# Kernel tuning notes

Measured on AMD Instinct MI355X. Metric: run time of the kernel, lower is better.

Reference implementation:

```python
import jax, jax.numpy as jnp
import numpy as np

B, T, D = 16, 512, 256
HH = D // 2   # per-direction hidden of bidirectional GRU
G, Z, R, NA = 32, 8, 16, 18


def _gru_step(h, x, wih, whh, bih, bhh):
    # torch.nn.GRUCell math
    gi = x @ wih.T + bih
    gh = h @ whh.T + bhh
    ir, iz, inn = jnp.split(gi, 3, axis=-1)
    hr, hz, hn = jnp.split(gh, 3, axis=-1)
    r = jax.nn.sigmoid(ir + hr)
    z = jax.nn.sigmoid(iz + hz)
    n = jnp.tanh(inn + r * hn)
    return (1.0 - z) * n + z * h


def _gru_seq(x_tbd, wih, whh, bih, bhh):
    h0 = jnp.zeros((x_tbd.shape[1], whh.shape[1]), x_tbd.dtype)
    def step(h, x):
        h = _gru_step(h, x, wih, whh, bih, bhh)
        return h, h
    _, hs = jax.lax.scan(step, h0, x_tbd)
    return hs  # (T, B, H)


def setup_inputs() -> dict:
    key = jax.random.key(0)
    ks = jax.random.split(key, 26)
    rn = lambda k, s, sc: jax.random.normal(k, s, jnp.float32) * sc
    d = {
        'e_seq': rn(ks[0], (B, T, D), 1.0),
        'eps':   rn(ks[1], (B, T, Z), 1.0),
        # acausal bidirectional GRU (fwd + bwd cells)
        'wih_f': rn(ks[2], (3 * HH, D), D ** -0.5),  'whh_f': rn(ks[3], (3 * HH, HH), HH ** -0.5),
        'bih_f': jnp.zeros((3 * HH,)), 'bhh_f': jnp.zeros((3 * HH,)),
        'wih_b': rn(ks[4], (3 * HH, D), D ** -0.5),  'whh_b': rn(ks[5], (3 * HH, HH), HH ** -0.5),
        'bih_b': jnp.zeros((3 * HH,)), 'bhh_b': jnp.zeros((3 * HH,)),
        # controller encoder GRUCell(2D -> G) + heads
        'wih_e': rn(ks[6], (3 * G, 2 * D), (2 * D) ** -0.5), 'whh_e': rn(ks[7], (3 * G, G), G ** -0.5),
        'bih_e': jnp.zeros((3 * G,)), 'bhh_e': jnp.zeros((3 * G,)),
        'mu_w': rn(ks[8], (Z, G), G ** -0.5),  'mu_b': jnp.zeros((Z,)),
        'lv_w': rn(ks[9], (Z, G), G ** -0.5),  'lv_b': jnp.zeros((Z,)),
        # switching unit MLP (D+G+Z -> 64 -> 1)
        'sw1_w': rn(ks[10], (64, D + G + Z), (D + G + Z) ** -0.5), 'sw1_b': jnp.zeros((64,)),
        'sw2_w': rn(ks[11], (1, 64), 64 ** -0.5), 'sw2_b': jnp.zeros((1,)),
        # decoder hypernet (Z -> 32 -> 2*D*R)
        'dec1_w': rn(ks[12], (32, Z), Z ** -0.5), 'dec1_b': jnp.zeros((32,)),
        'dec2_w': rn(ks[13], (2 * D * R, 32), 32 ** -0.5), 'dec2_b': jnp.zeros((2 * D * R,)),
        # final norm + action head
        'ln_g': jnp.ones((D,)), 'ln_b': jnp.zeros((D,)),
        'head_w': rn(ks[14], (NA, D), D ** -0.5), 'head_b': jnp.zeros((NA,)),
    }
    return d


def _forward(e_seq, eps, wih_f, whh_f, bih_f, bhh_f, wih_b, whh_b, bih_b, bhh_b,
             wih_e, whh_e, bih_e, bhh_e, mu_w, mu_b, lv_w, lv_b,
             sw1_w, sw1_b, sw2_w, sw2_b, dec1_w, dec1_b, dec2_w, dec2_b,
             ln_g, ln_b, head_w, head_b):
    Bz, Tt, Dm = e_seq.shape
    e_tbd = jnp.swapaxes(e_seq, 0, 1)                      # (T, B, D)
    # AcausalEmbedder: bidirectional GRU
    fwd = _gru_seq(e_tbd, wih_f, whh_f, bih_f, bhh_f)
    bwd = _gru_seq(e_tbd[::-1], wih_b, whh_b, bih_b, bhh_b)[::-1]
    s_tbd = jnp.concatenate([fwd, bwd], axis=-1)           # (T, B, D)
    eps_tbd = jnp.swapaxes(eps, 0, 1)

    h0 = jnp.zeros((Bz, whh_e.shape[1]), e_seq.dtype)
    z0 = jnp.zeros((Bz, mu_w.shape[0]), e_seq.dtype)

    def step(carry, xs):
        h, z_prev = carry
        e_t, s_t, eps_t = xs
        h = _gru_step(h, jnp.concatenate([e_t, s_t], axis=-1), wih_e, whh_e, bih_e, bhh_e)
        mu = h @ mu_w.T + mu_b
        logvar = h @ lv_w.T + lv_b
        # switching unit uses updated h (causal)
        hid = jnp.tanh(jnp.concatenate([e_t, h, z_prev], axis=-1) @ sw1_w.T + sw1_b)
        beta = jax.nn.sigmoid(hid @ sw2_w.T + sw2_b)       # (B, 1)
        z = beta * (mu + jnp.exp(0.5 * logvar) * eps_t) + (1.0 - beta) * z_prev
        return (h, jax.lax.stop_gradient(z)), (mu, logvar, beta, z)

    _, (mu_t, lv_t, be_t, z_t) = jax.lax.scan(step, (h0, z0), (e_tbd, s_tbd, eps_tbd))
    mu_seq = jnp.swapaxes(mu_t, 0, 1)
    logvar_seq = jnp.swapaxes(lv_t, 0, 1)
    beta_seq = jnp.swapaxes(be_t, 0, 1)
    z_seq = jnp.swapaxes(z_t, 0, 1)                        # (B, T, Z)

    # ControllerDecoder: z -> (A, Bm); apply U = A @ Bm^T without materializing U
    hmid = jnp.tanh(z_seq @ dec1_w.T + dec1_b)
    ab = hmid @ dec2_w.T + dec2_b                          # (B, T, 2*D*R)
    DR = ab.shape[-1] // 2
    A = ab[..., :DR].reshape(Bz, Tt, Dm, -1)               # (B, T, D, R)
    Bm = ab[..., DR:].reshape(Bz, Tt, Dm, -1)
    tmp = jnp.einsum('btdr,btd->btr', Bm, e_seq)
    perturbed = e_seq + jnp.einsum('btdr,btr->btd', A, tmp)

    # final LayerNorm + action head on obs positions
    mean = perturbed.mean(-1, keepdims=True)
    var = perturbed.var(-1, keepdims=True)
    xn = (perturbed - mean) * jax.lax.rsqrt(var + 1e-5) * ln_g + ln_b
    logits = xn @ head_w.T + head_b                        # (B, T, NA)
    return logits, mu_seq, logvar_seq, beta_seq, z_seq


def reference(e_seq, eps, wih_f, whh_f, bih_f, bhh_f, wih_b, whh_b, bih_b, bhh_b,
              wih_e, whh_e, bih_e, bhh_e, mu_w, mu_b, lv_w, lv_b,
              sw1_w, sw1_b, sw2_w, sw2_b, dec1_w, dec1_b, dec2_w, dec2_b,
              ln_g, ln_b, head_w, head_b):
    return _forward(e_seq, eps, wih_f, whh_f, bih_f, bhh_f, wih_b, whh_b, bih_b, bhh_b,
                    wih_e, whh_e, bih_e, bhh_e, mu_w, mu_b, lv_w, lv_b,
                    sw1_w, sw1_b, sw2_w, sw2_b, dec1_w, dec1_b, dec2_w, dec2_b,
                    ln_g, ln_b, head_w, head_b)
```

## Files before the change

### kernel.cpp

```cpp
#include <hip/hip_runtime.h>

#define TT 512
#define BB 16
#define DD 256
#define HHH 128
#define GG 32
#define ZZ 8
#define RR_ 16
#define NAA 18

typedef _Float16 h2v __attribute__((ext_vector_type(2)));
typedef __attribute__((ext_vector_type(4))) float f4;
typedef __attribute__((ext_vector_type(4))) int i4;

__device__ __forceinline__ float sigmoid_(float x) { return 1.f / (1.f + __expf(-x)); }
__device__ __forceinline__ float tanh_(float x) { float e = __expf(2.f * x); return 1.f - 2.f / (e + 1.f); }
__device__ __forceinline__ float dot4(float4 a, float4 b) {
    return a.x * b.x + a.y * b.y + a.z * b.z + a.w * b.w;
}
__device__ __forceinline__ h2v u2h2(unsigned u) { union { unsigned u; h2v h; } c; c.u = u; return c.h; }

__device__ __forceinline__ void lds_barrier() {
    asm volatile("s_waitcnt lgkmcnt(0)" ::: "memory");
    __builtin_amdgcn_s_barrier();
}

template <int CTRL, int RM, int BM, bool BC>
__device__ __forceinline__ float dpp_add_f(float v) {
    return v + __int_as_float(__builtin_amdgcn_update_dpp(0, __float_as_int(v), CTRL, RM, BM, BC));
}
__device__ __forceinline__ float wave_sum_bcast(float p) {
    p = dpp_add_f<0x111, 0xf, 0xf, true>(p);
    p = dpp_add_f<0x112, 0xf, 0xf, true>(p);
    p = dpp_add_f<0x114, 0xf, 0xf, true>(p);
    p = dpp_add_f<0x118, 0xf, 0xf, true>(p);
    p = dpp_add_f<0x142, 0xa, 0xf, false>(p);
    p = dpp_add_f<0x143, 0xc, 0xf, false>(p);
    return __int_as_float(__builtin_amdgcn_readlane(__float_as_int(p), 63));
}
__device__ __forceinline__ float quad_sum(float v) {
    v = dpp_add_f<0xB1, 0xf, 0xf, true>(v);
    v = dpp_add_f<0x4E, 0xf, 0xf, true>(v);
    return v;
}

__global__ __launch_bounds__(256) void pack_w(
    const float* __restrict__ wf, const float* __restrict__ wb,
    const float* __restrict__ we,
    unsigned* __restrict__ pk, unsigned* __restrict__ pk_e)
{
    int i = blockIdx.x * 256 + threadIdx.x;
    if (i < 49152) {
        int dir = i / 24576; int r = i % 24576;
        int w = r / 3072;    int r2 = r % 3072;
        int T = r2 / 1024;   int r3 = r2 % 1024;
        int kt = r3 / 256;   int r4 = r3 % 256;
        int lane = r4 / 4;   int jd = r4 % 4;
        const float* wsrc = dir ? wb : wf;
        int row = T * 128 + 16 * w + (lane & 15);
        int k0 = kt * 32 + (lane >> 4) * 8 + 2 * jd;
        union { _Float16 h[2]; unsigned u; } c;
        c.h[0] = (_Float16)wsrc[row * 128 + k0];
        c.h[1] = (_Float16)wsrc[row * 128 + k0 + 1];
        pk[i] = c.u;
    } else if (i < 50688) {
        int ie = i - 49152;
        int s = ie / 384;  int rem = ie % 384;
        int k = rem / 12;  int e = rem % 12;
        int j = e / 4;     int m = e % 4;
        int row = j * 32 + k, k0 = 8 * s + 2 * m;
        union { _Float16 h[2]; unsigned u; } c;
        c.h[0] = (_Float16)we[row * 32 + k0];
        c.h[1] = (_Float16)we[row * 32 + k0 + 1];
        pk_e[ie] = c.u;
    }
}

__global__ __launch_bounds__(256) void gemm_k(
    const float* __restrict__ A, int K, const float* __restrict__ W, int ldw,
    const float* __restrict__ bias, float* __restrict__ Out, int ldout, int N, int accFlag)
{
    __shared__ float At[64][36];
    __shared__ float Wt[32][36];
    int row0 = blockIdx.x * 64, n0 = blockIdx.y * 32;
    int tid = threadIdx.x;
    int tx = tid & 15, ty = tid >> 4;
    float acc[4][2] = {};
    for (int k0 = 0; k0 < K; k0 += 32) {
        #pragma unroll
        for (int i = 0; i < 8; ++i) {
            int idx = tid + i * 256; int rr = idx >> 5, kk = idx & 31;
            At[rr][kk] = A[(size_t)(row0 + rr) * K + k0 + kk];
        }
        #pragma unroll
        for (int i = 0; i < 4; ++i) {
            int idx = tid + i * 256; int nn = idx >> 5, kk = idx & 31;
            Wt[nn][kk] = (n0 + nn < N) ? W[(size_t)(n0 + nn) * ldw + k0 + kk] : 0.f;
        }
        __syncthreads();
        #pragma unroll
        for (int kk = 0; kk < 32; kk += 4) {
            float4 w0 = *(const float4*)&Wt[tx][kk];
            float4 w1 = *(const float4*)&Wt[tx + 16][kk];
            #pragma unroll
            for (int rr = 0; rr < 4; ++rr) {
                float4 av = *(const float4*)&At[ty * 4 + rr][kk];
                acc[rr][0] += dot4(av, w0);
                acc[rr][1] += dot4(av, w1);
            }
        }
        __syncthreads();
    }
    #pragma unroll
    for (int cc = 0; cc < 2; ++cc) {
        int n = n0 + tx + cc * 16;
        if (n < N) {
            float badd = bias ? bias[n] : 0.f;
            #pragma unroll
            for (int rr = 0; rr < 4; ++rr) {
                int row = row0 + ty * 4 + rr;
                float v = acc[rr][cc] + badd;
                if (accFlag) Out[(size_t)row * ldout + n] += v;
                else         Out[(size_t)row * ldout + n] = v;
            }
        }
    }
}

__global__ __launch_bounds__(256) void gemm_gi(
    const float* __restrict__ A,
    const float* __restrict__ wf, const float* __restrict__ bf, float* __restrict__ of,
    const float* __restrict__ wb, const float* __restrict__ bb, float* __restrict__ ob)
{
    __shared__ float At[64][36];
    __shared__ float Wt[32][36];
    int y = blockIdx.y;
    const float* W; const float* bias; float* Out; int n0;
    if (y < 12) { W = wf; bias = bf; Out = of; n0 = y * 32; }
    else        { W = wb; bias = bb; Out = ob; n0 = (y - 12) * 32; }
    int row0 = blockIdx.x * 64;
    int tid = threadIdx.x;
    int tx = tid & 15, ty = tid >> 4;
    float acc[4][2] = {};
    for (int k0 = 0; k0 < 256; k0 += 32) {
        #pragma unroll
        for (int i = 0; i < 8; ++i) {
            int idx = tid + i * 256; int rr = idx >> 5, kk = idx & 31;
            At[rr][kk] = A[(size_t)(row0 + rr) * 256 + k0 + kk];
        }
        #pragma unroll
        for (int i = 0; i < 4; ++i) {
            int idx = tid + i * 256; int nn = idx >> 5, kk = idx & 31;
            Wt[nn][kk] = W[(size_t)(n0 + nn) * 256 + k0 + kk];
        }
        __syncthreads();
        #pragma unroll
        for (int kk = 0; kk < 32; kk += 4) {
            float4 w0 = *(const float4*)&Wt[tx][kk];
            float4 w1 = *(const float4*)&Wt[tx + 16][kk];
            #pragma unroll
            for (int rr = 0; rr < 4; ++rr) {
                float4 av = *(const float4*)&At[ty * 4 + rr][kk];
                acc[rr][0] += dot4(av, w0);
                acc[rr][1] += dot4(av, w1);
            }
        }
        __syncthreads();
    }
    #pragma unroll
    for (int cc = 0; cc < 2; ++cc) {
        int n = n0 + tx + cc * 16;
        float badd = bias[n];
        #pragma unroll
        for (int rr = 0; rr < 4; ++rr) {
            int row = row0 + ty * 4 + rr;
            Out[(size_t)row * 384 + n] = acc[rr][cc] + badd;
        }
    }
}

struct __align__(16) SmGru { _Float16 hb[2][128]; };
struct __align__(16) SmGemm { float At[64][36]; float Wt[32][36]; };
union __align__(16) SmU { SmGru g; SmGemm m; };

__device__ __forceinline__ void gemm_tile512(
    const float* __restrict__ A, int K, const float* __restrict__ W, int ldw,
    const float* __restrict__ bias, float* __restrict__ Out, int ldout, int N,
    int row0, int n0, SmGemm& sm)
{
    int tid = threadIdx.x;
    int tx = tid & 31, ty = tid >> 5;
    float acc[4] = {};
    for (int k0 = 0; k0 < K; k0 += 32) {
        #pragma unroll
        for (int i = 0; i < 4; ++i) {
            int idx = tid + i * 512; int rr = idx >> 5, kk = idx & 31;
            sm.At[rr][kk] = A[(size_t)(row0 + rr) * K + k0 + kk];
        }
        #pragma unroll
        for (int i = 0; i < 2; ++i) {
            int idx = tid + i * 512; int nn = idx >> 5, kk = idx & 31;
            sm.Wt[nn][kk] = (n0 + nn < N) ? W[(size_t)(n0 + nn) * ldw + k0 + kk] : 0.f;
        }
        __syncthreads();
        #pragma unroll
        for (int kk = 0; kk < 32; kk += 4) {
            float4 w0 = *(const float4*)&sm.Wt[tx][kk];
            #pragma unroll
            for (int rr = 0; rr < 4; ++rr) {
                float4 av = *(const float4*)&sm.At[ty * 4 + rr][kk];
                acc[rr] += dot4(av, w0);
            }
        }
        __syncthreads();
    }
    int n = n0 + tx;
    if (n < N) {
        float badd = bias ? bias[n] : 0.f;
        #pragma unroll
        for (int rr = 0; rr < 4; ++rr)
            Out[(size_t)(row0 + ty * 4 + rr) * ldout + n] = acc[rr] + badd;
    }
}

__global__ __launch_bounds__(512, 2) void gru_fused(
    const float* __restrict__ gi_f, const float* __restrict__ gi_b,
    const unsigned* __restrict__ pk,
    const float* __restrict__ bhh_f, const float* __restrict__ bhh_b,
    float* __restrict__ s_seq,
    const float* __restrict__ e,
    const float* __restrict__ wih_e, const float* __restrict__ bih_e, float* __restrict__ gie,
    const float* __restrict__ sw1_w, const float* __restrict__ sw1_b, float* __restrict__ swe)
{
    __shared__ SmU sm;
    int bx = blockIdx.x;
    if (bx >= 416) {
        int t = bx - 416;
        gemm_tile512(e, 256, sw1_w, 296, sw1_b, swe, 64, 64, (t & 127) * 64, (t >> 7) * 32, sm.m);
        return;
    }
    if (bx >= 32) {
        int t = bx - 32;
        gemm_tile512(e, 256, wih_e, 512, bih_e, gie, 96, 96, (t & 127) * 64, (t >> 7) * 32, sm.m);
        return;
    }

    int dir = bx >> 4, b = bx & 15;
    const float* gi  = dir ? gi_b  : gi_f;
    const float* bhh = dir ? bhh_b : bhh_f;
    int tid = threadIdx.x;
    int w = tid >> 6;
    int lane = tid & 63;
    int quad = lane >> 4;
    int c = lane & 15;
    int j = 16 * w + c;

    i4 bf[3][4];
    #pragma unroll
    for (int T = 0; T < 3; ++T)
        #pragma unroll
        for (int kt = 0; kt < 4; ++kt)
            bf[T][kt] = *(const i4*)(pk + (size_t)((((dir * 8 + w) * 3 + T) * 4 + kt) * 64 + lane) * 4);
    #pragma unroll
    for (int T = 0; T < 3; ++T)
        #pragma unroll
        for (int kt = 0; kt < 4; ++kt)
            asm volatile("" : "+a"(bf[T][kt]));

    if (tid < 128) sm.g.hb[0][tid] = (_Float16)0.f;

    float bhr = 0.f, bhz = 0.f, bhn = 0.f;
    float gra = 0.f, gza = 0.f, gna = 0.f;
    float grb = 0.f, gzb = 0.f, gnb = 0.f;
    float hreg = 0.f;
    if (lane < 16) {
        bhr = bhh[j]; bhz = bhh[128 + j]; bhn = bhh[256 + j];
        int t0 = dir ? 511 : 0;
        int t1 = dir ? 510 : 1;
        size_t p0 = (size_t)(b * TT + t0) * 384;
        size_t p1 = (size_t)(b * TT + t1) * 384;
        gra = gi[p0 + j]; gza = gi[p0 + 128 + j]; gna = gi[p0 + 256 + j];
        grb = gi[p1 + j]; gzb = gi[p1 + 128 + j]; gnb = gi[p1 + 256 + j];
    }
    __syncthreads();

    int cur = 0;
    auto body = [&](int step, float& gr, float& gz, float& gn) {
        i4 af[4];
        #pragma unroll
        for (int kt = 0; kt < 4; ++kt)
            af[kt] = *(const i4*)(&sm.g.hb[cur][kt * 32 + quad * 8]);
        f4 accrA = {0.f, 0.f, 0.f, 0.f}, accrB = {0.f, 0.f, 0.f, 0.f};
        f4 acczA = {0.f, 0.f, 0.f, 0.f}, acczB = {0.f, 0.f, 0.f, 0.f};
        f4 accnA = {0.f, 0.f, 0.f, 0.f}, accnB = {0.f, 0.f, 0.f, 0.f};
        asm volatile("s_nop 3");
        asm volatile("v_mfma_f32_16x16x32_f16 %0, %1, %2, %0" : "+v"(accrA) : "v"(af[0]), "a"(bf[0][0]));
        asm volatile("v_mfma_f32_16x16x32_f16 %0, %1, %2, %0" : "+v"(acczA) : "v"(af[0]), "a"(bf[1][0]));
        asm volatile("v_mfma_f32_16x16x32_f16 %0, %1, %2, %0" : "+v"(accnA) : "v"(af[0]), "a"(bf[2][0]));
        asm volatile("v_mfma_f32_16x16x32_f16 %0, %1, %2, %0" : "+v"(accrB) : "v"(af[2]), "a"(bf[0][2]));
        asm volatile("v_mfma_f32_16x16x32_f16 %0, %1, %2, %0" : "+v"(acczB) : "v"(af[2]), "a"(bf[1][2]));
        asm volatile("v_mfma_f32_16x16x32_f16 %0, %1, %2, %0" : "+v"(accnB) : "v"(af[2]), "a"(bf[2][2]));
        asm volatile("v_mfma_f32_16x16x32_f16 %0, %1, %2, %0" : "+v"(accrA) : "v"(af[1]), "a"(bf[0][1]));
        asm volatile("v_mfma_f32_16x16x32_f16 %0, %1, %2, %0" : "+v"(acczA) : "v"(af[1]), "a"(bf[1][1]));
        asm volatile("v_mfma_f32_16x16x32_f16 %0, %1, %2, %0" : "+v"(accnA) : "v"(af[1]), "a"(bf[2][1]));
        asm volatile("v_mfma_f32_16x16x32_f16 %0, %1, %2, %0" : "+v"(accrB) : "v"(af[3]), "a"(bf[0][3]));
        asm volatile("v_mfma_f32_16x16x32_f16 %0, %1, %2, %0" : "+v"(acczB) : "v"(af[3]), "a"(bf[1][3]));
        asm volatile("v_mfma_f32_16x16x32_f16 %0, %1, %2, %0" : "+v"(accnB) : "v"(af[3]), "a"(bf[2][3]));
        asm volatile("s_nop 7\n\ts_nop 7");
        if (lane < 16) {
            int t = dir ? (511 - step) : step;
            int p = b * TT + t;
            float ar = accrA[0] + accrB[0];
            float az = acczA[0] + acczB[0];
            float an = accnA[0] + accnB[0];
            float r = sigmoid_(gr + bhr + ar);
            float z = sigmoid_(gz + bhz + az);
            float n = tanh_(gn + r * (bhn + an));
            float hn = (1.f - z) * n + z * hreg;
            hreg = hn;
            sm.g.hb[cur ^ 1][j] = (_Float16)hn;
            s_seq[(size_t)p * 256 + dir * 128 + j] = hn;
            int s2 = step + 2;
            int tp = (s2 < 512) ? (dir ? (511 - s2) : s2) : t;
            size_t p2 = (size_t)(b * TT + tp) * 384;
            gr = gi[p2 + j]; gz = gi[p2 + 128 + j]; gn = gi[p2 + 256 + j];
        }
        lds_barrier();
        cur ^= 1;
    };

    for (int step = 0; step < 512; step += 2) {
        body(step,     gra, gza, gna);
        body(step + 1, grb, gzb, gnb);
    }
}

__global__ __launch_bounds__(128, 1) void ctrl_fused(
    const float* __restrict__ gie, const unsigned* __restrict__ pk_e,
    const float* __restrict__ bhh_e,
    const float* __restrict__ mu_w, const float* __restrict__ mu_b,
    const float* __restrict__ lv_w, const float* __restrict__ lv_b,
    const float* __restrict__ sw1_w, const float* __restrict__ sw2_w,
    const float* __restrict__ sw2_b,
    const float* __restrict__ swe,
    const float* __restrict__ eps,
    float* __restrict__ out_mu, float* __restrict__ out_lv,
    float* __restrict__ beta_o, float* __restrict__ z_o)
{
    int b = blockIdx.x;
    int tid = threadIdx.x;
    int wid = tid >> 6;
    int lane = tid & 63;
    int pbase = b * TT;

    __shared__ __align__(16) _Float16 hb[2][32];
    __shared__ __align__(16) float    hf[2][32];
    __shared__ __align__(16) float    zc[8];

    int k = lane >> 1, s2 = lane & 1;
    unsigned wg[24];
    float bhr = 0.f, bhz = 0.f, bhn = 0.f, hreg = 0.f;
    float g1a = 0.f, g2a = 0.f, g3a = 0.f, g1b = 0.f, g2b = 0.f, g3b = 0.f;
    if (wid == 0) {
        #pragma unroll
        for (int ss = 0; ss < 2; ++ss) {
            const uint4* wp = (const uint4*)(pk_e + ((size_t)((2 * s2 + ss) * 32) + k) * 12);
            #pragma unroll
            for (int i = 0; i < 3; ++i) {
                uint4 u = wp[i];
                wg[12 * ss + 4 * i + 0] = u.x;
                wg[12 * ss + 4 * i + 1] = u.y;
                wg[12 * ss + 4 * i + 2] = u.z;
                wg[12 * ss + 4 * i + 3] = u.w;
            }
        }
        if (tid < 32) hb[0][tid] = (_Float16)0.f;
        if (s2 == 0) {
            bhr = bhh_e[k]; bhz = bhh_e[32 + k]; bhn = bhh_e[64 + k];
            size_t p0 = (size_t)pbase * 96, p1 = (size_t)(pbase + 1) * 96;
            g1a = gie[p0 + k]; g2a = gie[p0 + 32 + k]; g3a = gie[p0 + 64 + k];
            g1b = gie[p1 + k]; g2b = gie[p1 + 32 + k]; g3b = gie[p1 + 64 + k];
        }
    }

    int q = lane;
    int x = lane >> 3, kind = (lane >> 2) & 1, s = lane & 3;
    float swh[32], wz[8], mlw[8];
    float w2 = 0.f, sb2 = 0.f, mlb = 0.f;
    float zreg[8] = {0.f, 0.f, 0.f, 0.f, 0.f, 0.f, 0.f, 0.f};
    float hpa = 0.f, hpb = 0.f, epa = 0.f, epb = 0.f;
    if (wid == 1) {
        #pragma unroll
        for (int kk = 0; kk < 32; ++kk) swh[kk] = sw1_w[(size_t)q * 296 + 256 + kk];
        #pragma unroll
        for (int xx = 0; xx < 8; ++xx) wz[xx] = sw1_w[(size_t)q * 296 + 288 + xx];
        w2 = sw2_w[q];
        sb2 = sw2_b[0];
        const float* mw = kind ? lv_w : mu_w;
        #pragma unroll
        for (int m = 0; m < 8; ++m) mlw[m] = mw[x * 32 + 8 * s + m];
        mlb = kind ? lv_b[x] : mu_b[x];
        hpa = swe[(size_t)pbase * 64 + q];
        hpb = swe[(size_t)(pbase + 1) * 64 + q];
        epa = eps[(size_t)pbase * 8 + x];
        epb = eps[(size_t)(pbase + 1) * 8 + x];
    }
    __syncthreads();

    int cur = 0;

    auto prod = [&](int t, float& g1, float& g2, float& g3) {
        const uint4* hv = (const uint4*)(&hb[cur][16 * s2]);
        uint4 hA = hv[0], hB = hv[1];
        unsigned hw[8] = {hA.x, hA.y, hA.z, hA.w, hB.x, hB.y, hB.z, hB.w};
        float a0 = 0.f, a1 = 0.f, a2 = 0.f, c0 = 0.f, c1 = 0.f, c2 = 0.f;
        #pragma unroll
        for (int m = 0; m < 4; ++m) {
            a0 = __builtin_amdgcn_fdot2(u2h2(wg[m]),      u2h2(hw[m]),     a0, false);
            a1 = __builtin_amdgcn_fdot2(u2h2(wg[4 + m]),  u2h2(hw[m]),     a1, false);
            a2 = __builtin_amdgcn_fdot2(u2h2(wg[8 + m]),  u2h2(hw[m]),     a2, false);
            c0 = __builtin_amdgcn_fdot2(u2h2(wg[12 + m]), u2h2(hw[4 + m]), c0, false);
            c1 = __builtin_amdgcn_fdot2(u2h2(wg[16 + m]), u2h2(hw[4 + m]), c1, false);
            c2 = __builtin_amdgcn_fdot2(u2h2(wg[20 + m]), u2h2(hw[4 + m]), c2, false);
        }
        a0 += c0; a1 += c1; a2 += c2;
        a0 = dpp_add_f<0xB1, 0xf, 0xf, true>(a0);
        a1 = dpp_add_f<0xB1, 0xf, 0xf, true>(a1);
        a2 = dpp_add_f<0xB1, 0xf, 0xf, true>(a2);
        if (s2 == 0) {
            float r = sigmoid_(g1 + bhr + a0);
            float z = sigmoid_(g2 + bhz + a1);
            float n = tanh_(g3 + r * (bhn + a2));
            float hn = (1.f - z) * n + z * hreg;
            hreg = hn;
            hb[cur ^ 1][k] = (_Float16)hn;
            hf[cur ^ 1][k] = hn;
            int t2 = (t + 2 < 512) ? t + 2 : t;
            size_t p2 = (size_t)(pbase + t2) * 96;
            g1 = gie[p2 + k]; g2 = gie[p2 + 32 + k]; g3 = gie[p2 + 64 + k];
        }
    };

    auto cons = [&](int t, float& hp, float& ep) {
        const float4* hv4 = (const float4*)(&hf[cur][0]);
        float4 h4[8];
        #pragma unroll
        for (int i = 0; i < 8; ++i) h4[i] = hv4[i];
        float a = hp;
        #pragma unroll
        for (int xx = 0; xx < 8; ++xx) a += wz[xx] * zreg[xx];
        #pragma unroll
        for (int i = 0; i < 8; ++i) {
            a += swh[4 * i]     * h4[i].x;
            a += swh[4 * i + 1] * h4[i].y;
            a += swh[4 * i + 2] * h4[i].z;
            a += swh[4 * i + 3] * h4[i].w;
        }
        float hid = tanh_(a);
        float beta = sigmoid_(wave_sum_bcast(w2 * hid) + sb2);
        float4 hs0 = *(const float4*)(&hf[cur][8 * s]);
        float4 hs1 = *(const float4*)(&hf[cur][8 * s + 4]);
        float pacc = mlw[0] * hs0.x + mlw[1] * hs0.y + mlw[2] * hs0.z + mlw[3] * hs0.w
                   + mlw[4] * hs1.x + mlw[5] * hs1.y + mlw[6] * hs1.z + mlw[7] * hs1.w;
        pacc = quad_sum(pacc);
        float v = pacc + mlb;
        float other = __int_as_float(__builtin_amdgcn_ds_swizzle(__float_as_int(v), 0x101F));
        float muv = kind ? other : v;
        float lvv = kind ? v : other;
        float cand = muv + __expf(0.5f * lvv) * ep;
        if ((lane & 7) == 0) zc[x] = cand;
        asm volatile("s_waitcnt lgkmcnt(0)" ::: "memory");
        float4 cz0 = *(const float4*)&zc[0];
        float4 cz1 = *(const float4*)&zc[4];
        float omb = 1.f - beta;
        zreg[0] = beta * cz0.x + omb * zreg[0]; zreg[1] = beta * cz0.y + omb * zreg[1];
        zreg[2] = beta * cz0.z + omb * zreg[2]; zreg[3] = beta * cz0.w + omb * zreg[3];
        zreg[4] = beta * cz1.x + omb * zreg[4]; zreg[5] = beta * cz1.y + omb * zreg[5];
        zreg[6] = beta * cz1.z + omb * zreg[6]; zreg[7] = beta * cz1.w + omb * zreg[7];
        int p = pbase + t;
        if (lane == 0) {
            beta_o[p] = beta;
            *(float4*)(z_o + (size_t)p * 8)     = make_float4(zreg[0], zreg[1], zreg[2], zreg[3]);
            *(float4*)(z_o + (size_t)p * 8 + 4) = make_float4(zreg[4], zreg[5], zreg[6], zreg[7]);
        }
        if ((lane & 7) == 0) out_mu[(size_t)p * 8 + x] = muv;
        if ((lane & 7) == 4) out_lv[(size_t)p * 8 + x] = lvv;
        int t2 = (t + 2 < 512) ? t + 2 : t;
        hp = swe[(size_t)(pbase + t2) * 64 + q];
        ep = eps[(size_t)(pbase + t2) * 8 + x];
    };

    for (int it = 0; it < 512; it += 2) {
        if (wid == 0) prod(it, g1a, g2a, g3a);
        else if (it > 0) cons(it - 1, hpb, epb);
        lds_barrier();
        cur ^= 1;
        if (wid == 0) prod(it + 1, g1b, g2b, g3b);
        else cons(it, hpa, epa);
        lds_barrier();
        cur ^= 1;
    }
    if (wid == 1) cons(511, hpb, epb);
}

__global__ __launch_bounds__(256, 3) void decoder_final(
    const float* __restrict__ e_seq, const float* __restrict__ z_o,
    const float* __restrict__ dec1_w, const float* __restrict__ dec1_b,
    const float* __restrict__ dec2_w, const float* __restrict__ dec2_b,
    const float* __restrict__ ln_g, const float* __restrict__ ln_b,
    const float* __restrict__ head_w, const float* __restrict__ head_b,
    float* __restrict__ logits)
{
    __shared__ __align__(16) float e_l[8][256];
    __shared__ __align__(16) float hmid[8][32];
    __shared__ float zl[8][8];
    __shared__ float tmpw[8][16];
    __shared__ __align__(16) float partb[2048];
    __shared__ float red1[8][16];
    __shared__ float red2[8][16];
    __shared__ float stats[8][2];
    int tid = threadIdx.x;
    int p0 = blockIdx.x * 8;

    {
        const float4* eg = (const float4*)(e_seq + (size_t)p0 * 256);
        float4* el4 = (float4*)&e_l[0][0];
        el4[tid] = eg[tid];
        el4[tid + 256] = eg[tid + 256];
        if (tid < 64) ((float*)zl)[tid] = z_o[p0 * 8 + tid];
    }
    __syncthreads();
    {
        int pp = tid >> 5, g = tid & 31;
        float a = dec1_b[g];
        #pragma unroll
        for (int x = 0; x < 8; ++x) a += dec1_w[g * 8 + x] * zl[pp][x];
        hmid[pp][g] = tanh_(a);
    }
    __syncthreads();
    {
        int r = tid & 15, dgrp = tid >> 4;
        float acc[8];
        #pragma unroll
        for (int pp = 0; pp < 8; ++pp) acc[pp] = 0.f;
        for (int iblk = 0; iblk < 8; ++iblk) {
            float4 wr[2][8]; float wb[2]; int dd[2];
            #pragma unroll
            for (int ii = 0; ii < 2; ++ii) {
                int d = dgrp + 16 * (iblk * 2 + ii);
                dd[ii] = d;
                int row = 4096 + d * 16 + r;
                const float4* wp = (const float4*)(dec2_w + (size_t)row * 32);
                #pragma unroll
                for (int g = 0; g < 8; ++g) wr[ii][g] = wp[g];
                wb[ii] = dec2_b[row];
            }
            #pragma unroll 1
            for (int pp = 0; pp < 8; ++pp) {
                const float4* hv = (const float4*)hmid[pp];
                float b0 = wb[0], b1 = wb[1];
                #pragma unroll
                for (int g = 0; g < 8; ++g) {
                    float4 hh = hv[g];
                    b0 += dot4(wr[0][g], hh);
                    b1 += dot4(wr[1][g], hh);
                }
                acc[pp] += b0 * e_l[pp][dd[0]] + b1 * e_l[pp][dd[1]];
            }
        }
        #pragma unroll
        for (int pp = 0; pp < 8; ++pp) partb[(pp * 16 + r) * 16 + dgrp] = acc[pp];
    }
    __syncthreads();
    if (tid < 128) {
        int pp = tid >> 4, rr = tid & 15;
        float s = 0.f;
        #pragma unroll
        for (int dg = 0; dg < 16; ++dg) s += partb[(pp * 16 + rr) * 16 + dg];
        tmpw[pp][rr] = s;
    }
    __syncthreads();
    {
        int d = tid;
        float po[8];
        #pragma unroll
        for (int pp = 0; pp < 8; ++pp) po[pp] = e_l[pp][d];
        for (int rblk = 0; rblk < 8; ++rblk) {
            float4 wr[2][8]; float wb[2];
            #pragma unroll
            for (int ii = 0; ii < 2; ++ii) {
                int row = d * 16 + rblk * 2 + ii;
                const float4* wp = (const float4*)(dec2_w + (size_t)row * 32);
                #pragma unroll
                for (int g = 0; g < 8; ++g) wr[ii][g] = wp[g];
                wb[ii] = dec2_b[row];
            }
            #pragma unroll 1
            for (int pp = 0; pp < 8; ++pp) {
                const float4* hv = (const float4*)hmid[pp];
                float a0 = wb[0], a1 = wb[1];
                #pragma unroll
                for (int g = 0; g < 8; ++g) {
                    float4 hh = hv[g];
                    a0 += dot4(wr[0][g], hh);
                    a1 += dot4(wr[1][g], hh);
                }
                po[pp] += a0 * tmpw[pp][rblk * 2] + a1 * tmpw[pp][rblk * 2 + 1];
            }
        }
        #pragma unroll
        for (int pp = 0; pp < 8; ++pp) partb[pp * 256 + d] = po[pp];
    }
    __syncthreads();
    if (tid < 128) {
        int pp = tid >> 4, c = tid & 15;
        float s = 0.f, s2 = 0.f;
        #pragma unroll
        for (int i = 0; i < 16; ++i) { float v = partb[pp * 256 + c * 16 + i]; s += v; s2 += v * v; }
        red1[pp][c] = s; red2[pp][c] = s2;
    }
    __syncthreads();
    if (tid < 8) {
        float s = 0.f, s2 = 0.f;
        #pragma unroll
        for (int c = 0; c < 16; ++c) { s += red1[tid][c]; s2 += red2[tid][c]; }
        float mean = s * (1.f / 256.f);
        float var = s2 * (1.f / 256.f) - mean * mean;
        stats[tid][0] = mean;
        stats[tid][1] = rsqrtf(var + 1e-5f);
    }
    __syncthreads();
    {
        int d = tid;
        float g = ln_g[d], bln = ln_b[d];
        #pragma unroll
        for (int pp = 0; pp < 8; ++pp) {
            float v = (partb[pp * 256 + d] - stats[pp][0]) * stats[pp][1];
            partb[pp * 256 + d] = v * g + bln;
        }
    }
    __syncthreads();
    if (tid < 144) {
        int pp = tid / 18, na = tid - pp * 18;
        float a = head_b[na];
        for (int d2 = 0; d2 < 256; ++d2)
            a += partb[pp * 256 + d2] * head_w[na * 256 + d2];
        logits[(size_t)(p0 + pp) * 18 + na] = a;
    }
}

extern "C" void kernel_launch(void* const* d_in, const int* in_sizes, int n_in,
                              void* d_out, int out_size, void* d_ws, size_t ws_size,
                              hipStream_t stream) {
    (void)in_sizes; (void)n_in; (void)out_size; (void)ws_size;
    const float* e     = (const float*)d_in[0];
    const float* eps   = (const float*)d_in[1];
    const float* wih_f = (const float*)d_in[2];
    const float* whh_f = (const float*)d_in[3];
    const float* bih_f = (const float*)d_in[4];
    const float* bhh_f = (const float*)d_in[5];
    const float* wih_b = (const float*)d_in[6];
    const float* whh_b = (const float*)d_in[7];
    const float* bih_b = (const float*)d_in[8];
    const float* bhh_b = (const float*)d_in[9];
    const float* wih_e = (const float*)d_in[10];
    const float* whh_e = (const float*)d_in[11];
    const float* bih_e = (const float*)d_in[12];
    const float* bhh_e = (const float*)d_in[13];
    const float* mu_w  = (const float*)d_in[14];
    const float* mu_b  = (const float*)d_in[15];
    const float* lv_w  = (const float*)d_in[16];
    const float* lv_b  = (const float*)d_in[17];
    const float* sw1_w = (const float*)d_in[18];
    const float* sw1_b = (const float*)d_in[19];
    const float* sw2_w = (const float*)d_in[20];
    const float* sw2_b = (const float*)d_in[21];
    const float* dec1_w = (const float*)d_in[22];
    const float* dec1_b = (const float*)d_in[23];
    const float* dec2_w = (const float*)d_in[24];
    const float* dec2_b = (const float*)d_in[25];
    const float* ln_g  = (const float*)d_in[26];
    const float* ln_b  = (const float*)d_in[27];
    const float* head_w = (const float*)d_in[28];
    const float* head_b = (const float*)d_in[29];

    float* ws    = (float*)d_ws;
    float* gi_f  = ws;
    float* gi_b  = gi_f + 3145728;
    float* gie   = gi_b + 3145728;
    float* swe   = gie + 786432;
    float* s_seq = swe + 524288;
    float* h_seq = s_seq + 2097152;
    unsigned* pk   = (unsigned*)(h_seq + 262144);
    unsigned* pk_e = pk + 49152;
    (void)h_seq;

    float* out       = (float*)d_out;
    float* out_logit = out;
    float* out_mu    = out + 147456;
    float* out_lv    = out + 212992;
    float* out_beta  = out + 278528;
    float* out_z     = out + 286720;

    pack_w<<<198, 256, 0, stream>>>(whh_f, whh_b, whh_e, pk, pk_e);
    gemm_gi<<<dim3(128, 24), 256, 0, stream>>>(e, wih_f, bih_f, gi_f, wih_b, bih_b, gi_b);
    gru_fused<<<672, 512, 0, stream>>>(gi_f, gi_b, pk, bhh_f, bhh_b, s_seq,
                                       e, wih_e, bih_e, gie, sw1_w, sw1_b, swe);
    gemm_k<<<dim3(128, 3), 256, 0, stream>>>(s_seq, 256, wih_e + 256, 512, nullptr, gie, 96, 96, 1);
    ctrl_fused<<<16, 128, 0, stream>>>(gie, pk_e, bhh_e, mu_w, mu_b, lv_w, lv_b,
                                       sw1_w, sw2_w, sw2_b, swe, eps,
                                       out_mu, out_lv, out_beta, out_z);
    decoder_final<<<1024, 256, 0, stream>>>(e, out_z, dec1_w, dec1_b, dec2_w, dec2_b,
                                            ln_g, ln_b, head_w, head_b, out_logit);
}
```

Before: 1.005 ms.

## Batch four controller steps per barrier with an 8-slot hidden-state ring

```diff
diff --git a/kernel.cpp b/kernel.cpp
--- a/kernel.cpp
+++ b/kernel.cpp
@@ -42,6 +42,9 @@
     v = dpp_add_f<0xB1, 0xf, 0xf, true>(v);
     v = dpp_add_f<0x4E, 0xf, 0xf, true>(v);
     return v;
+}
+__device__ __forceinline__ float rdlane(float v, int l) {
+    return __int_as_float(__builtin_amdgcn_readlane(__float_as_int(v), l));
 }
 
 __global__ __launch_bounds__(256) void pack_w(
@@ -353,14 +356,13 @@
     int lane = tid & 63;
     int pbase = b * TT;
 
-    __shared__ __align__(16) _Float16 hb[2][32];
-    __shared__ __align__(16) float    hf[2][32];
-    __shared__ __align__(16) float    zc[8];
+    __shared__ __align__(16) _Float16 hb[8][32];
+    __shared__ __align__(16) float    hf[8][32];
 
     int k = lane >> 1, s2 = lane & 1;
     unsigned wg[24];
     float bhr = 0.f, bhz = 0.f, bhn = 0.f, hreg = 0.f;
-    float g1a = 0.f, g2a = 0.f, g3a = 0.f, g1b = 0.f, g2b = 0.f, g3b = 0.f;
+    float g1[4] = {}, g2[4] = {}, g3[4] = {};
     if (wid == 0) {
         #pragma unroll
         for (int ss = 0; ss < 2; ++ss) {
@@ -374,43 +376,45 @@
                 wg[12 * ss + 4 * i + 3] = u.w;
             }
         }
-        if (tid < 32) hb[0][tid] = (_Float16)0.f;
+        if (lane < 32) hb[7][lane] = (_Float16)0.f;
         if (s2 == 0) {
             bhr = bhh_e[k]; bhz = bhh_e[32 + k]; bhn = bhh_e[64 + k];
-            size_t p0 = (size_t)pbase * 96, p1 = (size_t)(pbase + 1) * 96;
-            g1a = gie[p0 + k]; g2a = gie[p0 + 32 + k]; g3a = gie[p0 + 64 + k];
-            g1b = gie[p1 + k]; g2b = gie[p1 + 32 + k]; g3b = gie[p1 + 64 + k];
-        }
-    }
-
-    int q = lane;
+            #pragma unroll
+            for (int i = 0; i < 4; ++i) {
+                size_t p = (size_t)(pbase + i) * 96;
+                g1[i] = gie[p + k]; g2[i] = gie[p + 32 + k]; g3[i] = gie[p + 64 + k];
+            }
+        }
+    }
+
     int x = lane >> 3, kind = (lane >> 2) & 1, s = lane & 3;
-    float swh[32], wz[8], mlw[8];
+    float4 swh4[8];
+    float4 wz0v = {0,0,0,0}, wz1v = {0,0,0,0}, mlw0 = {0,0,0,0}, mlw1 = {0,0,0,0};
     float w2 = 0.f, sb2 = 0.f, mlb = 0.f;
-    float zreg[8] = {0.f, 0.f, 0.f, 0.f, 0.f, 0.f, 0.f, 0.f};
-    float hpa = 0.f, hpb = 0.f, epa = 0.f, epb = 0.f;
+    float4 zr0 = {0.f, 0.f, 0.f, 0.f}, zr1 = {0.f, 0.f, 0.f, 0.f};
+    float hp[4] = {}, ep[4] = {};
     if (wid == 1) {
         #pragma unroll
-        for (int kk = 0; kk < 32; ++kk) swh[kk] = sw1_w[(size_t)q * 296 + 256 + kk];
-        #pragma unroll
-        for (int xx = 0; xx < 8; ++xx) wz[xx] = sw1_w[(size_t)q * 296 + 288 + xx];
-        w2 = sw2_w[q];
+        for (int i = 0; i < 8; ++i)
+            swh4[i] = *(const float4*)(sw1_w + (size_t)lane * 296 + 256 + 4 * i);
+        wz0v = *(const float4*)(sw1_w + (size_t)lane * 296 + 288);
+        wz1v = *(const float4*)(sw1_w + (size_t)lane * 296 + 292);
+        w2 = sw2_w[lane];
         sb2 = sw2_b[0];
         const float* mw = kind ? lv_w : mu_w;
-        #pragma unroll
-        for (int m = 0; m < 8; ++m) mlw[m] = mw[x * 32 + 8 * s + m];
+        mlw0 = *(const float4*)(mw + x * 32 + 8 * s);
+        mlw1 = *(const float4*)(mw + x * 32 + 8 * s + 4);
         mlb = kind ? lv_b[x] : mu_b[x];
-        hpa = swe[(size_t)pbase * 64 + q];
-        hpb = swe[(size_t)(pbase + 1) * 64 + q];
-        epa = eps[(size_t)pbase * 8 + x];
-        epb = eps[(size_t)(pbase + 1) * 8 + x];
-    }
-    __syncthreads();
-
-    int cur = 0;
-
-    auto prod = [&](int t, float& g1, float& g2, float& g3) {
-        const uint4* hv = (const uint4*)(&hb[cur][16 * s2]);
+        #pragma unroll
+        for (int i = 0; i < 4; ++i) {
+            hp[i] = swe[(size_t)(pbase + i) * 64 + lane];
+            ep[i] = eps[(size_t)(pbase + i) * 8 + x];
+        }
+    }
+    __syncthreads();
+
+    auto prod_step = [&](int t, float& ga, float& gb, float& gc) {
+        const uint4* hv = (const uint4*)(&hb[(t - 1) & 7][16 * s2]);
         uint4 hA = hv[0], hB = hv[1];
         unsigned hw[8] = {hA.x, hA.y, hA.z, hA.w, hB.x, hB.y, hB.z, hB.w};
         float a0 = 0.f, a1 = 0.f, a2 = 0.f, c0 = 0.f, c1 = 0.f, c2 = 0.f;
@@ -428,79 +432,83 @@
         a1 = dpp_add_f<0xB1, 0xf, 0xf, true>(a1);
         a2 = dpp_add_f<0xB1, 0xf, 0xf, true>(a2);
         if (s2 == 0) {
-            float r = sigmoid_(g1 + bhr + a0);
-            float z = sigmoid_(g2 + bhz + a1);
-            float n = tanh_(g3 + r * (bhn + a2));
+            float r = sigmoid_(ga + bhr + a0);
+            float z = sigmoid_(gb + bhz + a1);
+            float n = tanh_(gc + r * (bhn + a2));
             float hn = (1.f - z) * n + z * hreg;
             hreg = hn;
-            hb[cur ^ 1][k] = (_Float16)hn;
-            hf[cur ^ 1][k] = hn;
-            int t2 = (t + 2 < 512) ? t + 2 : t;
-            size_t p2 = (size_t)(pbase + t2) * 96;
-            g1 = gie[p2 + k]; g2 = gie[p2 + 32 + k]; g3 = gie[p2 + 64 + k];
+            hb[t & 7][k] = (_Float16)hn;
+            hf[t & 7][k] = hn;
+            int t4 = (t + 4 < 512) ? (t + 4) : t;
+            size_t p2 = (size_t)(pbase + t4) * 96;
+            ga = gie[p2 + k]; gb = gie[p2 + 32 + k]; gc = gie[p2 + 64 + k];
         }
     };
 
-    auto cons = [&](int t, float& hp, float& ep) {
-        const float4* hv4 = (const float4*)(&hf[cur][0]);
-        float4 h4[8];
-        #pragma unroll
-        for (int i = 0; i < 8; ++i) h4[i] = hv4[i];
-        float a = hp;
-        #pragma unroll
-        for (int xx = 0; xx < 8; ++xx) a += wz[xx] * zreg[xx];
-        #pragma unroll
-        for (int i = 0; i < 8; ++i) {
-            a += swh[4 * i]     * h4[i].x;
-            a += swh[4 * i + 1] * h4[i].y;
-            a += swh[4 * i + 2] * h4[i].z;
-            a += swh[4 * i + 3] * h4[i].w;
-        }
-        float hid = tanh_(a);
-        float beta = sigmoid_(wave_sum_bcast(w2 * hid) + sb2);
-        float4 hs0 = *(const float4*)(&hf[cur][8 * s]);
-        float4 hs1 = *(const float4*)(&hf[cur][8 * s + 4]);
-        float pacc = mlw[0] * hs0.x + mlw[1] * hs0.y + mlw[2] * hs0.z + mlw[3] * hs0.w
-                   + mlw[4] * hs1.x + mlw[5] * hs1.y + mlw[6] * hs1.z + mlw[7] * hs1.w;
-        pacc = quad_sum(pacc);
+    auto cons_step = [&](int t, float& hpi, float& epi) {
+        int sl = t & 7;
+        const float4* hv4 = (const float4*)(&hf[sl][0]);
+        float4 h0 = hv4[0], h1 = hv4[1], h2 = hv4[2], h3 = hv4[3];
+        float4 h4 = hv4[4], h5 = hv4[5], h6 = hv4[6], h7 = hv4[7];
+        float d0 = dot4(swh4[0], h0) + dot4(swh4[1], h1);
+        float d1 = dot4(swh4[2], h2) + dot4(swh4[3], h3);
+        float d2 = dot4(swh4[4], h4) + dot4(swh4[5], h5);
+        float d3 = dot4(swh4[6], h6) + dot4(swh4[7], h7);
+        float hsum = (d0 + d1) + (d2 + d3);
+        float4 hs0 = *(const float4*)(&hf[sl][8 * s]);
+        float4 hs1 = *(const float4*)(&hf[sl][8 * s + 4]);
+        float pacc = quad_sum(dot4(mlw0, hs0) + dot4(mlw1, hs1));
         float v = pacc + mlb;
         float other = __int_as_float(__builtin_amdgcn_ds_swizzle(__float_as_int(v), 0x101F));
         float muv = kind ? other : v;
         float lvv = kind ? v : other;
-        float cand = muv + __expf(0.5f * lvv) * ep;
-        if ((lane & 7) == 0) zc[x] = cand;
-        asm volatile("s_waitcnt lgkmcnt(0)" ::: "memory");
-        float4 cz0 = *(const float4*)&zc[0];
-        float4 cz1 = *(const float4*)&zc[4];
+        float cand = muv + __expf(0.5f * lvv) * epi;
+        float sc0 = rdlane(cand, 0),  sc1 = rdlane(cand, 8);
+        float sc2 = rdlane(cand, 16), sc3 = rdlane(cand, 24);
+        float sc4 = rdlane(cand, 32), sc5 = rdlane(cand, 40);
+        float sc6 = rdlane(cand, 48), sc7 = rdlane(cand, 56);
+        float az = dot4(wz0v, zr0) + dot4(wz1v, zr1);
+        float a = (hpi + hsum) + az;
+        float hid = tanh_(a);
+        float beta = sigmoid_(wave_sum_bcast(w2 * hid) + sb2);
         float omb = 1.f - beta;
-        zreg[0] = beta * cz0.x + omb * zreg[0]; zreg[1] = beta * cz0.y + omb * zreg[1];
-        zreg[2] = beta * cz0.z + omb * zreg[2]; zreg[3] = beta * cz0.w + omb * zreg[3];
-        zreg[4] = beta * cz1.x + omb * zreg[4]; zreg[5] = beta * cz1.y + omb * zreg[5];
-        zreg[6] = beta * cz1.z + omb * zreg[6]; zreg[7] = beta * cz1.w + omb * zreg[7];
+        zr0.x = beta * sc0 + omb * zr0.x; zr0.y = beta * sc1 + omb * zr0.y;
+        zr0.z = beta * sc2 + omb * zr0.z; zr0.w = beta * sc3 + omb * zr0.w;
+        zr1.x = beta * sc4 + omb * zr1.x; zr1.y = beta * sc5 + omb * zr1.y;
+        zr1.z = beta * sc6 + omb * zr1.z; zr1.w = beta * sc7 + omb * zr1.w;
         int p = pbase + t;
         if (lane == 0) {
             beta_o[p] = beta;
-            *(float4*)(z_o + (size_t)p * 8)     = make_float4(zreg[0], zreg[1], zreg[2], zreg[3]);
-            *(float4*)(z_o + (size_t)p * 8 + 4) = make_float4(zreg[4], zreg[5], zreg[6], zreg[7]);
+            *(float4*)(z_o + (size_t)p * 8)     = zr0;
+            *(float4*)(z_o + (size_t)p * 8 + 4) = zr1;
         }
         if ((lane & 7) == 0) out_mu[(size_t)p * 8 + x] = muv;
         if ((lane & 7) == 4) out_lv[(size_t)p * 8 + x] = lvv;
-        int t2 = (t + 2 < 512) ? t + 2 : t;
-        hp = swe[(size_t)(pbase + t2) * 64 + q];
-        ep = eps[(size_t)(pbase + t2) * 8 + x];
+        int t4 = (t + 4 < 512) ? (t + 4) : t;
+        hpi = swe[(size_t)(pbase + t4) * 64 + lane];
+        epi = eps[(size_t)(pbase + t4) * 8 + x];
     };
 
-    for (int it = 0; it < 512; it += 2) {
-        if (wid == 0) prod(it, g1a, g2a, g3a);
-        else if (it > 0) cons(it - 1, hpb, epb);
+    for (int ph = 0; ph < 129; ++ph) {
+        if (wid == 0) {
+            if (ph < 128) {
+                int t0 = ph * 4;
+                prod_step(t0,     g1[0], g2[0], g3[0]);
+                prod_step(t0 + 1, g1[1], g2[1], g3[1]);
+                prod_step(t0 + 2, g1[2], g2[2], g3[2]);
+                prod_step(t0 + 3, g1[3], g2[3], g3[3]);
+            }
+        } else {
+            if (ph >= 1) {
+                int t0 = (ph - 1) * 4;
+                cons_step(t0,     hp[0], ep[0]);
+                cons_step(t0 + 1, hp[1], ep[1]);
+                cons_step(t0 + 2, hp[2], ep[2]);
+                cons_step(t0 + 3, hp[3], ep[3]);
+            }
+        }
         lds_barrier();
-        cur ^= 1;
-        if (wid == 0) prod(it + 1, g1b, g2b, g3b);
-        else cons(it, hpa, epa);
-        lds_barrier();
-        cur ^= 1;
-    }
-    if (wid == 1) cons(511, hpb, epb);
+    }
 }
 
 __global__ __launch_bounds__(256, 3) void decoder_final(
```

Measured after the change: 918.5 us. 8.6% less time.
